# Optimization experiments

Hardware: AMD Instinct MI355X
Metric: run time of the kernel (lower is better)

Reference implementation:

```python
import jax, jax.numpy as jnp
import numpy as np

M_FUZZ = 2.0        # self.m
EPSILON = 1e-8      # self.Epsilon
MAX_ITER = 25       # self.max_iterion


def setup_inputs() -> dict:
    key = jax.random.key(0)
    k1, k2 = jax.random.split(key)
    data = jax.random.normal(k1, (300000, 64), dtype=jnp.float32)
    u0_raw = jax.random.uniform(k2, (300000, 64), dtype=jnp.float32)
    return {"data": data, "u0_raw": u0_raw, "cluster": 64}


def reference(data, u0_raw, cluster):
    # Fuzzy c-means, faithful to GranularComputing.forward:
    #   iterate: C = center(U); U = update(U, C); C_new = center(U);
    #            stop if ||C_new - C||_F < Epsilon; return C (pre-update center).
    m = M_FUZZ
    p = 2.0 / (m - 1.0)  # exponent in membership update (== 2.0)
    N, D = data.shape

    # initialize_matrix_U: random rows normalized to sum to 1
    U0 = u0_raw / jnp.sum(u0_raw, axis=1, keepdims=True)  # [N, c]

    def center(U):
        Um = U ** m                                        # [N, c]
        num = Um.T @ data                                  # [c, D]
        den = jnp.sum(Um, axis=0)[:, None]                 # [c, 1]
        return num / den

    x2 = jnp.sum(data * data, axis=1, keepdims=True)       # [N, 1]

    def sqdist(C):
        # squared Euclidean distances [N, c] via expansion (no N x c x D tensor)
        c2 = jnp.sum(C * C, axis=1)                        # [c]
        return jnp.maximum(x2 + c2 - 2.0 * (data @ C.T), 0.0)

    def step(carry, _):
        U, C_ret, done = carry
        C = center(U)                                      # [c, D]
        # u_ij = 1 / sum_k (d_ij / d_ik)^p  ==  d_ij^{-p} / sum_k d_ik^{-p}
        w = sqdist(C) ** (-p / 2.0)                        # [N, c]
        U_new = w / jnp.sum(w, axis=1, keepdims=True)
        C_new = center(U_new)
        diff = jnp.sqrt(jnp.sum((C_new - C) ** 2))
        # freeze state after convergence (emulates the early break)
        U_out = jnp.where(done, U, U_new)
        C_out = jnp.where(done, C_ret, C)
        return (U_out, C_out, done | (diff < EPSILON)), None

    C0 = jnp.zeros((cluster, D), dtype=data.dtype)
    (_, V, _), _ = jax.lax.scan(
        step, (U0, C0, jnp.array(False)), None, length=MAX_ITER + 1
    )
    return V  # [cluster, D]
```

## Files before the change

kernel.cpp:

```cpp
#include <hip/hip_runtime.h>


#define DM 64
#define CL 64
#define PARTIAL_STRIDE 4160
#define MAX_ITER 25
#define MAX_BLOCKS 512
#define LDP 72

typedef __attribute__((ext_vector_type(8))) short bf16x8;
typedef __attribute__((ext_vector_type(4))) float f32x4;

__device__ __forceinline__ unsigned f2bf1(float f) {
  unsigned u = __builtin_bit_cast(unsigned, f);
  return (u + 0x7FFFu + ((u >> 16) & 1u)) >> 16;
}
__device__ __forceinline__ unsigned pkbf(float a, float b) {
  return f2bf1(a) | (f2bf1(b) << 16);
}

__device__ __forceinline__ float wave_sum(float v) {
#define DPPADD(ctrl, rmask)                                                  \
  v += __builtin_bit_cast(float, __builtin_amdgcn_update_dpp(                \
           0, __builtin_bit_cast(int, v), ctrl, rmask, 0xf, false));
  DPPADD(0x111, 0xf)
  DPPADD(0x112, 0xf)
  DPPADD(0x114, 0xf)
  DPPADD(0x118, 0xf)
  DPPADD(0x142, 0xa)
  DPPADD(0x143, 0xc)
#undef DPPADD
  return __builtin_bit_cast(
      float, __builtin_amdgcn_readlane(__builtin_bit_cast(int, v), 63));
}

__device__ __forceinline__ float group16_sum(float v) {
#define DPPADD(ctrl)                                                         \
  v += __builtin_bit_cast(float, __builtin_amdgcn_update_dpp(                \
           0, __builtin_bit_cast(int, v), ctrl, 0xf, 0xf, false));
  DPPADD(0xB1)
  DPPADD(0x4E)
  DPPADD(0x141)
  DPPADD(0x140)
#undef DPPADD
  return v;
}

__global__ void fcm_prep(const float* __restrict__ data, float* __restrict__ x2,
                         unsigned short* __restrict__ xbf,
                         float* __restrict__ diffac, int* __restrict__ done,
                         int* __restrict__ ticket, int N) {
  int i = blockIdx.x * blockDim.x + threadIdx.x;
  if (i == 0) { *diffac = 0.0f; *done = 0; *ticket = 0; }
  if (i < N) {
    const float4* r = (const float4*)(data + (size_t)i * DM);
    unsigned short* xo = xbf + (size_t)i * DM;
    float s = 0.0f;
#pragma unroll
    for (int q = 0; q < DM / 4; q++) {
      float4 v = r[q];
      s = fmaf(v.x, v.x, s); s = fmaf(v.y, v.y, s);
      s = fmaf(v.z, v.z, s); s = fmaf(v.w, v.w, s);
      uint2 pk = {pkbf(v.x, v.y), pkbf(v.z, v.w)};
      *(uint2*)(void*)(xo + q * 4) = pk;
    }
    x2[i] = s;
  }
}

template <bool INIT>
__global__ __launch_bounds__(256, 3)
void fcm_pass(const unsigned short* __restrict__ xbf, const float* __restrict__ x2,
              const float* __restrict__ CU,
              float* __restrict__ partial, const int* __restrict__ done,
              int N, int ntiles) {
  if (!INIT && *done) return;
  __shared__ __align__(16) unsigned short Xb[64 * LDP];
  __shared__ __align__(16) unsigned short XTb[64 * LDP];
  __shared__ __align__(16) unsigned short umT[64 * LDP];
  __shared__ __align__(16) float rpart[4 * 64];
  __shared__ __align__(16) float rrs[64];
  __shared__ __align__(16) float x2s[64];

  const int tid  = threadIdx.x;
  const int w    = __builtin_amdgcn_readfirstlane(tid >> 6);
  const int col  = tid & 15;
  const int quad = (tid >> 4) & 3;

  bf16x8 cf0, cf1;
  float c2j = 0.0f;
  if (!INIT) {
    const float* crow = CU + (size_t)(16 * w + col) * DM;
    float4 ca = *(const float4*)(crow + quad * 8);
    float4 cb = *(const float4*)(crow + quad * 8 + 4);
    float4 cc = *(const float4*)(crow + 32 + quad * 8);
    float4 cd = *(const float4*)(crow + 32 + quad * 8 + 4);
    float cp = ca.x*ca.x + ca.y*ca.y + ca.z*ca.z + ca.w*ca.w
             + cb.x*cb.x + cb.y*cb.y + cb.z*cb.z + cb.w*cb.w
             + cc.x*cc.x + cc.y*cc.y + cc.z*cc.z + cc.w*cc.w
             + cd.x*cd.x + cd.y*cd.y + cd.z*cd.z + cd.w*cd.w;
    cp += __shfl_xor(cp, 16, 64);
    cp += __shfl_xor(cp, 32, 64);
    c2j = cp;
    union { bf16x8 v; unsigned u[4]; } P0, P1;
    P0.u[0] = pkbf(ca.x, ca.y); P0.u[1] = pkbf(ca.z, ca.w);
    P0.u[2] = pkbf(cb.x, cb.y); P0.u[3] = pkbf(cb.z, cb.w);
    P1.u[0] = pkbf(cc.x, cc.y); P1.u[1] = pkbf(cc.z, cc.w);
    P1.u[2] = pkbf(cd.x, cd.y); P1.u[3] = pkbf(cd.z, cd.w);
    cf0 = P0.v; cf1 = P1.v;
  }

  f32x4 D2[4];
#pragma unroll
  for (int dt = 0; dt < 4; dt++) D2[dt] = f32x4{0.f, 0.f, 0.f, 0.f};
  float den = 0.0f;

  for (int t = blockIdx.x; t < ntiles; t += gridDim.x) {
    const int base = t * 64;
    const int np = min(64, N - base);
    __syncthreads();

    for (int i = tid; i < 512; i += 256) {
      int p = i >> 3;
      int d8 = (i & 7) * 8;
      bf16x8 v = bf16x8{0, 0, 0, 0, 0, 0, 0, 0};
      if (p < np) v = *(const bf16x8*)(xbf + (size_t)(base + p) * DM + d8);
      *(bf16x8*)(void*)&Xb[p * LDP + d8] = v;
#pragma unroll
      for (int k = 0; k < 8; k++)
        XTb[(d8 + k) * LDP + p] = (unsigned short)v[k];
    }
    if (tid < 64) x2s[tid] = (base + tid < N) ? x2[base + tid] : 0.0f;
    __syncthreads();

    float W[4][4];
    if (INIT) {
#pragma unroll
      for (int pt = 0; pt < 4; pt++)
#pragma unroll
        for (int r = 0; r < 4; r++) {
          int pl = pt * 16 + quad * 4 + r;
          W[pt][r] = (pl < np)
              ? CU[(size_t)(base + pl) * CL + 16 * w + col] : 0.0f;
        }
    } else {
#pragma unroll
      for (int pt = 0; pt < 4; pt++) {
        bf16x8 a0 = *(const bf16x8*)(const void*)&Xb[(pt * 16 + col) * LDP + quad * 8];
        bf16x8 a1 = *(const bf16x8*)(const void*)&Xb[(pt * 16 + col) * LDP + 32 + quad * 8];
        f32x4 s = f32x4{0.f, 0.f, 0.f, 0.f};
        s = __builtin_amdgcn_mfma_f32_16x16x32_bf16(a0, cf0, s, 0, 0, 0);
        s = __builtin_amdgcn_mfma_f32_16x16x32_bf16(a1, cf1, s, 0, 0, 0);
        f32x4 x2v = *(const f32x4*)(const void*)&x2s[pt * 16 + quad * 4];
#pragma unroll
        for (int r = 0; r < 4; r++) {
          float dist = fmaxf(fmaf(-2.0f, s[r], x2v[r] + c2j), 0.0f);
          W[pt][r] = __builtin_amdgcn_rcpf(dist);
        }
      }
    }

    float rs[4][4];
#pragma unroll
    for (int pt = 0; pt < 4; pt++)
#pragma unroll
      for (int r = 0; r < 4; r++) rs[pt][r] = group16_sum(W[pt][r]);
    if (col == 0) {
#pragma unroll
      for (int pt = 0; pt < 4; pt++) {
        float4 v4 = {rs[pt][0], rs[pt][1], rs[pt][2], rs[pt][3]};
        *(float4*)(void*)&rpart[w * 64 + pt * 16 + quad * 4] = v4;
      }
    }
    __syncthreads();
    if (tid < 64) {
      float rt = rpart[tid] + rpart[64 + tid] + rpart[128 + tid] + rpart[192 + tid];
      rrs[tid] = __builtin_amdgcn_rcpf(rt);
    }
    __syncthreads();

#pragma unroll
    for (int pt = 0; pt < 4; pt++) {
      f32x4 rrv = *(const f32x4*)(const void*)&rrs[pt * 16 + quad * 4];
      float um[4];
#pragma unroll
      for (int r = 0; r < 4; r++) {
        float u = W[pt][r] * rrv[r];
        float m = u * u;
        um[r] = (pt * 16 + quad * 4 + r < np) ? m : 0.0f;
        den += um[r];
      }
      unsigned long long w64 = (unsigned long long)pkbf(um[0], um[1]) |
                               ((unsigned long long)pkbf(um[2], um[3]) << 32);
      *(unsigned long long*)(void*)&umT[(16 * w + col) * LDP + pt * 16 + quad * 4] = w64;
    }

#pragma unroll
    for (int pb = 0; pb < 2; pb++) {
      bf16x8 au = *(const bf16x8*)(const void*)&umT[(16 * w + col) * LDP + pb * 32 + quad * 8];
#pragma unroll
      for (int dt = 0; dt < 4; dt++) {
        bf16x8 bx = *(const bf16x8*)(const void*)&XTb[(dt * 16 + col) * LDP + pb * 32 + quad * 8];
        D2[dt] = __builtin_amdgcn_mfma_f32_16x16x32_bf16(au, bx, D2[dt], 0, 0, 0);
      }
    }
  }

  den += __shfl_xor(den, 16, 64);
  den += __shfl_xor(den, 32, 64);
  float* pb = partial + (size_t)blockIdx.x * PARTIAL_STRIDE;
  if (quad == 0) pb[CL * DM + 16 * w + col] = den;
#pragma unroll
  for (int dt = 0; dt < 4; dt++)
#pragma unroll
    for (int r = 0; r < 4; r++)
      pb[(size_t)(16 * w + quad * 4 + r) * DM + dt * 16 + col] = D2[dt][r];
}

__global__ __launch_bounds__(1024, 1)
void fcm_reduce(const float* __restrict__ partial, float* __restrict__ Cnew,
                const float* __restrict__ Cold, float* __restrict__ out,
                float* __restrict__ diffac, int* __restrict__ done,
                int* __restrict__ ticket, int compute_diff, int nb) {
  if (compute_diff && *done) return;
  __shared__ float sm[16 * 64];
  __shared__ float sden[1024];
  __shared__ int lastflag;
  __shared__ float sdiff;
  int j = blockIdx.x;
  int tid = threadIdx.x;
  int d = tid & 63;
  int slice = tid >> 6;
  float s = 0.0f;
  for (int b = slice; b < nb; b += 16)
    s += partial[(size_t)b * PARTIAL_STRIDE + j * DM + d];
  sm[slice * 64 + d] = s;
  float dv = 0.0f;
  for (int b = tid; b < nb; b += 1024)
    dv += partial[(size_t)b * PARTIAL_STRIDE + CL * DM + j];
  sden[tid] = dv;
  __syncthreads();
#pragma unroll
  for (int st = 8; st; st >>= 1) {
    if (slice < st) sm[slice * 64 + d] += sm[(slice + st) * 64 + d];
    __syncthreads();
  }
#pragma unroll
  for (int st = 512; st >= 64; st >>= 1) {
    if (tid < st) sden[tid] += sden[tid + st];
    __syncthreads();
  }
  if (tid < 64) {
    float denj = wave_sum(sden[tid]);
    float c = sm[tid] / denj;
    Cnew[j * DM + tid] = c;
    if (compute_diff) {
      float df = c - Cold[j * DM + tid];
      float tot = wave_sum(df * df);
      if (tid == 0) atomicAdd(diffac, tot);
    }
  }
  if (!compute_diff) return;
  __syncthreads();
  if (tid == 0) {
    __threadfence();
    int t = atomicAdd(ticket, 1);
    lastflag = (t == (int)gridDim.x - 1);
  }
  __syncthreads();
  if (!lastflag) return;
  if (tid == 0) sdiff = atomicAdd(diffac, 0.0f);
  __syncthreads();
  if (sdiff < 1e-16f) {
    for (int i = tid; i < CL * DM; i += 1024) out[i] = Cold[i];
    if (tid == 0) *done = 1;
  }
  if (tid == 0) { *diffac = 0.0f; *ticket = 0; }
}

__global__ void fcm_final(const float* __restrict__ Clast, float* __restrict__ out,
                          const int* __restrict__ done) {
  if (*done) return;
  int i = blockIdx.x * blockDim.x + threadIdx.x;
  if (i < CL * DM) out[i] = Clast[i];
}

extern "C" void kernel_launch(void* const* d_in, const int* in_sizes, int n_in,
                              void* d_out, int out_size, void* d_ws, size_t ws_size,
                              hipStream_t stream) {
  const float* data = (const float*)d_in[0];
  const float* u0   = (const float*)d_in[1];
  float* out = (float*)d_out;
  int N = in_sizes[0] / DM;
  int ntiles = (N + 63) / 64;

  float* ws = (float*)d_ws;
  size_t Noff = ((size_t)N + 15) & ~(size_t)15;
  float* x2 = ws;
  unsigned short* xbf = (unsigned short*)(ws + Noff);
  float* C0 = ws + Noff + (size_t)N * 32;
  float* C1 = C0 + CL * DM;
  float* diffac = C1 + CL * DM;
  int* done = (int*)(diffac + 1);
  int* ticket = (int*)(diffac + 2);
  float* partial = diffac + 16;

  size_t used = Noff + (size_t)N * 32 + 2 * CL * DM + 16;
  size_t avail = (ws_size / 4 > used) ? (ws_size / 4 - used) / PARTIAL_STRIDE : 0;
  int nb = (int)(avail < MAX_BLOCKS ? avail : MAX_BLOCKS);
  if (nb < 1) nb = 1;

  hipLaunchKernelGGL(fcm_prep, dim3((N + 255) / 256), dim3(256), 0, stream,
                     data, x2, xbf, diffac, done, ticket, N);
  hipLaunchKernelGGL((fcm_pass<true>), dim3(nb), dim3(256), 0, stream,
                     xbf, x2, u0, partial, done, N, ntiles);
  hipLaunchKernelGGL(fcm_reduce, dim3(64), dim3(1024), 0, stream,
                     partial, C0, C1, out, diffac, done, ticket, 0, nb);

  float* bufs[2] = {C0, C1};
  for (int k = 0; k < MAX_ITER; k++) {
    float* Cc = bufs[k & 1];
    float* Cn = bufs[(k + 1) & 1];
    hipLaunchKernelGGL((fcm_pass<false>), dim3(nb), dim3(256), 0, stream,
                       xbf, x2, Cc, partial, done, N, ntiles);
    hipLaunchKernelGGL(fcm_reduce, dim3(64), dim3(1024), 0, stream,
                       partial, Cn, Cc, out, diffac, done, ticket, 1, nb);
  }
  hipLaunchKernelGGL(fcm_final, dim3(16), dim3(256), 0, stream,
                     bufs[1], out, done);
}
```

Baseline: 427.1 us.

## Accumulate centers with global atomics and collapse reduce into single-block finalize

Each pass block now atomically adds its partial numerator and denominator sums into one shared accumulator, replacing the per-block partial buffers and the 64-block tree reduction with ticket counter. A one-block finalize divides, zeroes the accumulator, computes the convergence diff and writes the output on the last iteration, which also removes the separate final kernel. The prep kernel is reworked to 16 threads per row with a group reduction, and the transposed LDS tile is built from paired 32-bit loads instead of scalar 16-bit stores. The cost is atomic contention (512 blocks × 4160 atomics per pass) and nondeterministic float summation order.

Measured after the change: 1.635 ms. +282.8%, slower.

```diff
diff --git a/kernel.cpp b/kernel.cpp
--- a/kernel.cpp
+++ b/kernel.cpp
@@ -3,9 +3,8 @@
 
 #define DM 64
 #define CL 64
-#define PARTIAL_STRIDE 4160
 #define MAX_ITER 25
-#define MAX_BLOCKS 512
+#define NB 512
 #define LDP 72
 
 typedef __attribute__((ext_vector_type(8))) short bf16x8;
@@ -47,24 +46,20 @@
 }
 
 __global__ void fcm_prep(const float* __restrict__ data, float* __restrict__ x2,
-                         unsigned short* __restrict__ xbf,
-                         float* __restrict__ diffac, int* __restrict__ done,
-                         int* __restrict__ ticket, int N) {
-  int i = blockIdx.x * blockDim.x + threadIdx.x;
-  if (i == 0) { *diffac = 0.0f; *done = 0; *ticket = 0; }
-  if (i < N) {
-    const float4* r = (const float4*)(data + (size_t)i * DM);
-    unsigned short* xo = xbf + (size_t)i * DM;
-    float s = 0.0f;
-#pragma unroll
-    for (int q = 0; q < DM / 4; q++) {
-      float4 v = r[q];
-      s = fmaf(v.x, v.x, s); s = fmaf(v.y, v.y, s);
-      s = fmaf(v.z, v.z, s); s = fmaf(v.w, v.w, s);
-      uint2 pk = {pkbf(v.x, v.y), pkbf(v.z, v.w)};
-      *(uint2*)(void*)(xo + q * 4) = pk;
-    }
-    x2[i] = s;
+                         unsigned short* __restrict__ xbf, float* __restrict__ acc,
+                         int* __restrict__ done, int N) {
+  int g = blockIdx.x * blockDim.x + threadIdx.x;
+  if (g < CL * DM + CL) acc[g] = 0.0f;
+  if (g == CL * DM + CL) *done = 0;
+  int row = g >> 4;
+  int c = g & 15;
+  if (row < N) {
+    float4 v = *(const float4*)(data + (size_t)row * DM + c * 4);
+    float s = fmaf(v.x, v.x, fmaf(v.y, v.y, fmaf(v.z, v.z, v.w * v.w)));
+    s = group16_sum(s);
+    if (c == 0) x2[row] = s;
+    uint2 pk = {pkbf(v.x, v.y), pkbf(v.z, v.w)};
+    *(uint2*)(void*)(xbf + (size_t)row * DM + c * 4) = pk;
   }
 }
 
@@ -72,7 +67,7 @@
 __global__ __launch_bounds__(256, 3)
 void fcm_pass(const unsigned short* __restrict__ xbf, const float* __restrict__ x2,
               const float* __restrict__ CU,
-              float* __restrict__ partial, const int* __restrict__ done,
+              float* __restrict__ acc, const int* __restrict__ done,
               int N, int ntiles) {
   if (!INIT && *done) return;
   __shared__ __align__(16) unsigned short Xb[64 * LDP];
@@ -126,9 +121,19 @@
       bf16x8 v = bf16x8{0, 0, 0, 0, 0, 0, 0, 0};
       if (p < np) v = *(const bf16x8*)(xbf + (size_t)(base + p) * DM + d8);
       *(bf16x8*)(void*)&Xb[p * LDP + d8] = v;
-#pragma unroll
-      for (int k = 0; k < 8; k++)
-        XTb[(d8 + k) * LDP + p] = (unsigned short)v[k];
+    }
+#pragma unroll
+    for (int it = 0; it < 4; it++) {
+      int idx = it * 256 + tid;
+      int d = (idx >> 5) * 2;
+      int p = (idx & 31) * 2;
+      unsigned w0 = 0, w1 = 0;
+      if (p < np)     w0 = *(const unsigned*)(xbf + (size_t)(base + p) * DM + d);
+      if (p + 1 < np) w1 = *(const unsigned*)(xbf + (size_t)(base + p + 1) * DM + d);
+      unsigned t0 = (w0 & 0xFFFFu) | (w1 << 16);
+      unsigned t1 = (w0 >> 16) | (w1 & 0xFFFF0000u);
+      *(unsigned*)(void*)&XTb[d * LDP + p] = t0;
+      *(unsigned*)(void*)&XTb[(d + 1) * LDP + p] = t1;
     }
     if (tid < 64) x2s[tid] = (base + tid < N) ? x2[base + tid] : 0.0f;
     __syncthreads();
@@ -208,81 +213,48 @@
 
   den += __shfl_xor(den, 16, 64);
   den += __shfl_xor(den, 32, 64);
-  float* pb = partial + (size_t)blockIdx.x * PARTIAL_STRIDE;
-  if (quad == 0) pb[CL * DM + 16 * w + col] = den;
+  if (quad == 0) atomicAdd(&acc[CL * DM + 16 * w + col], den);
 #pragma unroll
   for (int dt = 0; dt < 4; dt++)
 #pragma unroll
     for (int r = 0; r < 4; r++)
-      pb[(size_t)(16 * w + quad * 4 + r) * DM + dt * 16 + col] = D2[dt][r];
-}
-
-__global__ __launch_bounds__(1024, 1)
-void fcm_reduce(const float* __restrict__ partial, float* __restrict__ Cnew,
-                const float* __restrict__ Cold, float* __restrict__ out,
-                float* __restrict__ diffac, int* __restrict__ done,
-                int* __restrict__ ticket, int compute_diff, int nb) {
+      atomicAdd(&acc[(size_t)(16 * w + quad * 4 + r) * DM + dt * 16 + col], D2[dt][r]);
+}
+
+__global__ __launch_bounds__(256)
+void fcm_finalize(float* __restrict__ acc, float* __restrict__ Cnew,
+                  const float* __restrict__ Cold, float* __restrict__ out,
+                  int* __restrict__ done, int compute_diff, int last) {
   if (compute_diff && *done) return;
-  __shared__ float sm[16 * 64];
-  __shared__ float sden[1024];
-  __shared__ int lastflag;
+  __shared__ float sden[64];
+  __shared__ float sdf[4];
   __shared__ float sdiff;
-  int j = blockIdx.x;
   int tid = threadIdx.x;
-  int d = tid & 63;
-  int slice = tid >> 6;
-  float s = 0.0f;
-  for (int b = slice; b < nb; b += 16)
-    s += partial[(size_t)b * PARTIAL_STRIDE + j * DM + d];
-  sm[slice * 64 + d] = s;
-  float dv = 0.0f;
-  for (int b = tid; b < nb; b += 1024)
-    dv += partial[(size_t)b * PARTIAL_STRIDE + CL * DM + j];
-  sden[tid] = dv;
+  if (tid < 64) { sden[tid] = acc[CL * DM + tid]; acc[CL * DM + tid] = 0.0f; }
   __syncthreads();
-#pragma unroll
-  for (int st = 8; st; st >>= 1) {
-    if (slice < st) sm[slice * 64 + d] += sm[(slice + st) * 64 + d];
-    __syncthreads();
-  }
-#pragma unroll
-  for (int st = 512; st >= 64; st >>= 1) {
-    if (tid < st) sden[tid] += sden[tid + st];
-    __syncthreads();
-  }
-  if (tid < 64) {
-    float denj = wave_sum(sden[tid]);
-    float c = sm[tid] / denj;
-    Cnew[j * DM + tid] = c;
-    if (compute_diff) {
-      float df = c - Cold[j * DM + tid];
-      float tot = wave_sum(df * df);
-      if (tid == 0) atomicAdd(diffac, tot);
-    }
+  float dsum = 0.0f;
+#pragma unroll
+  for (int q = 0; q < 16; q++) {
+    int idx = q * 256 + tid;
+    float c = acc[idx] / sden[idx >> 6];
+    acc[idx] = 0.0f;
+    Cnew[idx] = c;
+    if (compute_diff) { float df = c - Cold[idx]; dsum = fmaf(df, df, dsum); }
   }
   if (!compute_diff) return;
+  dsum = wave_sum(dsum);
+  if ((tid & 63) == 0) sdf[tid >> 6] = dsum;
   __syncthreads();
-  if (tid == 0) {
-    __threadfence();
-    int t = atomicAdd(ticket, 1);
-    lastflag = (t == (int)gridDim.x - 1);
-  }
-  __syncthreads();
-  if (!lastflag) return;
-  if (tid == 0) sdiff = atomicAdd(diffac, 0.0f);
+  if (tid == 0) sdiff = (sdf[0] + sdf[1]) + (sdf[2] + sdf[3]);
   __syncthreads();
   if (sdiff < 1e-16f) {
-    for (int i = tid; i < CL * DM; i += 1024) out[i] = Cold[i];
+#pragma unroll
+    for (int q = 0; q < 16; q++) out[q * 256 + tid] = Cold[q * 256 + tid];
     if (tid == 0) *done = 1;
-  }
-  if (tid == 0) { *diffac = 0.0f; *ticket = 0; }
-}
-
-__global__ void fcm_final(const float* __restrict__ Clast, float* __restrict__ out,
-                          const int* __restrict__ done) {
-  if (*done) return;
-  int i = blockIdx.x * blockDim.x + threadIdx.x;
-  if (i < CL * DM) out[i] = Clast[i];
+  } else if (last) {
+#pragma unroll
+    for (int q = 0; q < 16; q++) out[q * 256 + tid] = Cnew[q * 256 + tid];
+  }
 }
 
 extern "C" void kernel_launch(void* const* d_in, const int* in_sizes, int n_in,
@@ -300,32 +272,23 @@
   unsigned short* xbf = (unsigned short*)(ws + Noff);
   float* C0 = ws + Noff + (size_t)N * 32;
   float* C1 = C0 + CL * DM;
-  float* diffac = C1 + CL * DM;
-  int* done = (int*)(diffac + 1);
-  int* ticket = (int*)(diffac + 2);
-  float* partial = diffac + 16;
-
-  size_t used = Noff + (size_t)N * 32 + 2 * CL * DM + 16;
-  size_t avail = (ws_size / 4 > used) ? (ws_size / 4 - used) / PARTIAL_STRIDE : 0;
-  int nb = (int)(avail < MAX_BLOCKS ? avail : MAX_BLOCKS);
-  if (nb < 1) nb = 1;
-
-  hipLaunchKernelGGL(fcm_prep, dim3((N + 255) / 256), dim3(256), 0, stream,
-                     data, x2, xbf, diffac, done, ticket, N);
-  hipLaunchKernelGGL((fcm_pass<true>), dim3(nb), dim3(256), 0, stream,
-                     xbf, x2, u0, partial, done, N, ntiles);
-  hipLaunchKernelGGL(fcm_reduce, dim3(64), dim3(1024), 0, stream,
-                     partial, C0, C1, out, diffac, done, ticket, 0, nb);
+  float* acc = C1 + CL * DM;
+  int* done = (int*)(acc + CL * DM + CL);
+
+  hipLaunchKernelGGL(fcm_prep, dim3((N * 16 + 255) / 256), dim3(256), 0, stream,
+                     data, x2, xbf, acc, done, N);
+  hipLaunchKernelGGL((fcm_pass<true>), dim3(NB), dim3(256), 0, stream,
+                     xbf, x2, u0, acc, done, N, ntiles);
+  hipLaunchKernelGGL(fcm_finalize, dim3(1), dim3(256), 0, stream,
+                     acc, C0, C1, out, done, 0, 0);
 
   float* bufs[2] = {C0, C1};
   for (int k = 0; k < MAX_ITER; k++) {
     float* Cc = bufs[k & 1];
     float* Cn = bufs[(k + 1) & 1];
-    hipLaunchKernelGGL((fcm_pass<false>), dim3(nb), dim3(256), 0, stream,
-                       xbf, x2, Cc, partial, done, N, ntiles);
-    hipLaunchKernelGGL(fcm_reduce, dim3(64), dim3(1024), 0, stream,
-                       partial, Cn, Cc, out, diffac, done, ticket, 1, nb);
-  }
-  hipLaunchKernelGGL(fcm_final, dim3(16), dim3(256), 0, stream,
-                     bufs[1], out, done);
-}
+    hipLaunchKernelGGL((fcm_pass<false>), dim3(NB), dim3(256), 0, stream,
+                       xbf, x2, Cc, acc, done, N, ntiles);
+    hipLaunchKernelGGL(fcm_finalize, dim3(1), dim3(256), 0, stream,
+                       acc, Cn, Cc, out, done, 1, (k == MAX_ITER - 1) ? 1 : 0);
+  }
+}
```

## Remap waves to point rows to drop cross-wave row-sum sync; coalesce prep and transpose

Applied to the files above, without the earlier changes.

Each wave now owns 16 data points and all 64 clusters, holding all four centroid fragments in registers. The membership row sum can then be reduced inside the wave, which removes the shared-memory rpart/rrs round trip and two block barriers per tile. The XT transpose is rebuilt with paired 32-bit loads and stores in place of scalar 16-bit scattered writes. The prep kernel uses 16 threads per row for coalesced access, and the grid cap grows to 768 blocks. In exchange each thread holds more registers for the centroid fragments, which may reduce occupancy.

Result: no change. 430.3 us (+0.8%).

```diff
diff --git a/kernel.cpp b/kernel.cpp
--- a/kernel.cpp
+++ b/kernel.cpp
@@ -5,7 +5,7 @@
 #define CL 64
 #define PARTIAL_STRIDE 4160
 #define MAX_ITER 25
-#define MAX_BLOCKS 512
+#define MAX_BLOCKS 768
 #define LDP 72
 
 typedef __attribute__((ext_vector_type(8))) short bf16x8;
@@ -47,24 +47,19 @@
 }
 
 __global__ void fcm_prep(const float* __restrict__ data, float* __restrict__ x2,
-                         unsigned short* __restrict__ xbf,
-                         float* __restrict__ diffac, int* __restrict__ done,
-                         int* __restrict__ ticket, int N) {
-  int i = blockIdx.x * blockDim.x + threadIdx.x;
-  if (i == 0) { *diffac = 0.0f; *done = 0; *ticket = 0; }
-  if (i < N) {
-    const float4* r = (const float4*)(data + (size_t)i * DM);
-    unsigned short* xo = xbf + (size_t)i * DM;
-    float s = 0.0f;
-#pragma unroll
-    for (int q = 0; q < DM / 4; q++) {
-      float4 v = r[q];
-      s = fmaf(v.x, v.x, s); s = fmaf(v.y, v.y, s);
-      s = fmaf(v.z, v.z, s); s = fmaf(v.w, v.w, s);
-      uint2 pk = {pkbf(v.x, v.y), pkbf(v.z, v.w)};
-      *(uint2*)(void*)(xo + q * 4) = pk;
-    }
-    x2[i] = s;
+                         unsigned short* __restrict__ xbf, float* __restrict__ diffac,
+                         int* __restrict__ done, int* __restrict__ ticket, int N) {
+  int g = blockIdx.x * blockDim.x + threadIdx.x;
+  if (g == 0) { *diffac = 0.0f; *done = 0; *ticket = 0; }
+  int row = g >> 4;
+  int c = g & 15;
+  if (row < N) {
+    float4 v = *(const float4*)(data + (size_t)row * DM + c * 4);
+    float s = fmaf(v.x, v.x, fmaf(v.y, v.y, fmaf(v.z, v.z, v.w * v.w)));
+    s = group16_sum(s);
+    if (c == 0) x2[row] = s;
+    uint2 pk = {pkbf(v.x, v.y), pkbf(v.z, v.w)};
+    *(uint2*)(void*)(xbf + (size_t)row * DM + c * 4) = pk;
   }
 }
 
@@ -79,7 +74,6 @@
   __shared__ __align__(16) unsigned short XTb[64 * LDP];
   __shared__ __align__(16) unsigned short umT[64 * LDP];
   __shared__ __align__(16) float rpart[4 * 64];
-  __shared__ __align__(16) float rrs[64];
   __shared__ __align__(16) float x2s[64];
 
   const int tid  = threadIdx.x;
@@ -87,33 +81,36 @@
   const int col  = tid & 15;
   const int quad = (tid >> 4) & 3;
 
-  bf16x8 cf0, cf1;
-  float c2j = 0.0f;
+  bf16x8 cf[4][2];
+  float c2v[4];
   if (!INIT) {
-    const float* crow = CU + (size_t)(16 * w + col) * DM;
-    float4 ca = *(const float4*)(crow + quad * 8);
-    float4 cb = *(const float4*)(crow + quad * 8 + 4);
-    float4 cc = *(const float4*)(crow + 32 + quad * 8);
-    float4 cd = *(const float4*)(crow + 32 + quad * 8 + 4);
-    float cp = ca.x*ca.x + ca.y*ca.y + ca.z*ca.z + ca.w*ca.w
-             + cb.x*cb.x + cb.y*cb.y + cb.z*cb.z + cb.w*cb.w
-             + cc.x*cc.x + cc.y*cc.y + cc.z*cc.z + cc.w*cc.w
-             + cd.x*cd.x + cd.y*cd.y + cd.z*cd.z + cd.w*cd.w;
-    cp += __shfl_xor(cp, 16, 64);
-    cp += __shfl_xor(cp, 32, 64);
-    c2j = cp;
-    union { bf16x8 v; unsigned u[4]; } P0, P1;
-    P0.u[0] = pkbf(ca.x, ca.y); P0.u[1] = pkbf(ca.z, ca.w);
-    P0.u[2] = pkbf(cb.x, cb.y); P0.u[3] = pkbf(cb.z, cb.w);
-    P1.u[0] = pkbf(cc.x, cc.y); P1.u[1] = pkbf(cc.z, cc.w);
-    P1.u[2] = pkbf(cd.x, cd.y); P1.u[3] = pkbf(cd.z, cd.w);
-    cf0 = P0.v; cf1 = P1.v;
+#pragma unroll
+    for (int g = 0; g < 4; g++) {
+      const float* crow = CU + (size_t)(g * 16 + col) * DM;
+      float4 ca = *(const float4*)(crow + quad * 8);
+      float4 cb = *(const float4*)(crow + quad * 8 + 4);
+      float4 cc = *(const float4*)(crow + 32 + quad * 8);
+      float4 cd = *(const float4*)(crow + 32 + quad * 8 + 4);
+      float cp = ca.x*ca.x + ca.y*ca.y + ca.z*ca.z + ca.w*ca.w
+               + cb.x*cb.x + cb.y*cb.y + cb.z*cb.z + cb.w*cb.w
+               + cc.x*cc.x + cc.y*cc.y + cc.z*cc.z + cc.w*cc.w
+               + cd.x*cd.x + cd.y*cd.y + cd.z*cd.z + cd.w*cd.w;
+      cp += __shfl_xor(cp, 16, 64);
+      cp += __shfl_xor(cp, 32, 64);
+      c2v[g] = cp;
+      union { bf16x8 v; unsigned u[4]; } P0, P1;
+      P0.u[0] = pkbf(ca.x, ca.y); P0.u[1] = pkbf(ca.z, ca.w);
+      P0.u[2] = pkbf(cb.x, cb.y); P0.u[3] = pkbf(cb.z, cb.w);
+      P1.u[0] = pkbf(cc.x, cc.y); P1.u[1] = pkbf(cc.z, cc.w);
+      P1.u[2] = pkbf(cd.x, cd.y); P1.u[3] = pkbf(cd.z, cd.w);
+      cf[g][0] = P0.v; cf[g][1] = P1.v;
+    }
   }
 
   f32x4 D2[4];
 #pragma unroll
   for (int dt = 0; dt < 4; dt++) D2[dt] = f32x4{0.f, 0.f, 0.f, 0.f};
-  float den = 0.0f;
+  float denacc[4] = {0.f, 0.f, 0.f, 0.f};
 
   for (int t = blockIdx.x; t < ntiles; t += gridDim.x) {
     const int base = t * 64;
@@ -126,9 +123,19 @@
       bf16x8 v = bf16x8{0, 0, 0, 0, 0, 0, 0, 0};
       if (p < np) v = *(const bf16x8*)(xbf + (size_t)(base + p) * DM + d8);
       *(bf16x8*)(void*)&Xb[p * LDP + d8] = v;
-#pragma unroll
-      for (int k = 0; k < 8; k++)
-        XTb[(d8 + k) * LDP + p] = (unsigned short)v[k];
+    }
+#pragma unroll
+    for (int it = 0; it < 4; it++) {
+      int idx = it * 256 + tid;
+      int d = (idx >> 5) * 2;
+      int p = (idx & 31) * 2;
+      unsigned w0 = 0, w1 = 0;
+      if (p < np)     w0 = *(const unsigned*)(xbf + (size_t)(base + p) * DM + d);
+      if (p + 1 < np) w1 = *(const unsigned*)(xbf + (size_t)(base + p + 1) * DM + d);
+      unsigned t0 = (w0 & 0xFFFFu) | (w1 << 16);
+      unsigned t1 = (w0 >> 16) | (w1 & 0xFFFF0000u);
+      *(unsigned*)(void*)&XTb[d * LDP + p] = t0;
+      *(unsigned*)(void*)&XTb[(d + 1) * LDP + p] = t1;
     }
     if (tid < 64) x2s[tid] = (base + tid < N) ? x2[base + tid] : 0.0f;
     __syncthreads();
@@ -136,64 +143,52 @@
     float W[4][4];
     if (INIT) {
 #pragma unroll
-      for (int pt = 0; pt < 4; pt++)
+      for (int g = 0; g < 4; g++)
 #pragma unroll
         for (int r = 0; r < 4; r++) {
-          int pl = pt * 16 + quad * 4 + r;
-          W[pt][r] = (pl < np)
-              ? CU[(size_t)(base + pl) * CL + 16 * w + col] : 0.0f;
+          int pl = 16 * w + quad * 4 + r;
+          W[g][r] = (pl < np)
+              ? CU[(size_t)(base + pl) * CL + g * 16 + col] : 0.0f;
         }
     } else {
-#pragma unroll
-      for (int pt = 0; pt < 4; pt++) {
-        bf16x8 a0 = *(const bf16x8*)(const void*)&Xb[(pt * 16 + col) * LDP + quad * 8];
-        bf16x8 a1 = *(const bf16x8*)(const void*)&Xb[(pt * 16 + col) * LDP + 32 + quad * 8];
+      bf16x8 a0 = *(const bf16x8*)(const void*)&Xb[(16 * w + col) * LDP + quad * 8];
+      bf16x8 a1 = *(const bf16x8*)(const void*)&Xb[(16 * w + col) * LDP + 32 + quad * 8];
+      f32x4 x2v = *(const f32x4*)(const void*)&x2s[16 * w + quad * 4];
+#pragma unroll
+      for (int g = 0; g < 4; g++) {
         f32x4 s = f32x4{0.f, 0.f, 0.f, 0.f};
-        s = __builtin_amdgcn_mfma_f32_16x16x32_bf16(a0, cf0, s, 0, 0, 0);
-        s = __builtin_amdgcn_mfma_f32_16x16x32_bf16(a1, cf1, s, 0, 0, 0);
-        f32x4 x2v = *(const f32x4*)(const void*)&x2s[pt * 16 + quad * 4];
+        s = __builtin_amdgcn_mfma_f32_16x16x32_bf16(a0, cf[g][0], s, 0, 0, 0);
+        s = __builtin_amdgcn_mfma_f32_16x16x32_bf16(a1, cf[g][1], s, 0, 0, 0);
 #pragma unroll
         for (int r = 0; r < 4; r++) {
-          float dist = fmaxf(fmaf(-2.0f, s[r], x2v[r] + c2j), 0.0f);
-          W[pt][r] = __builtin_amdgcn_rcpf(dist);
+          float dist = fmaxf(fmaf(-2.0f, s[r], x2v[r] + c2v[g]), 0.0f);
+          W[g][r] = __builtin_amdgcn_rcpf(dist);
         }
       }
     }
 
-    float rs[4][4];
-#pragma unroll
-    for (int pt = 0; pt < 4; pt++)
-#pragma unroll
-      for (int r = 0; r < 4; r++) rs[pt][r] = group16_sum(W[pt][r]);
-    if (col == 0) {
-#pragma unroll
-      for (int pt = 0; pt < 4; pt++) {
-        float4 v4 = {rs[pt][0], rs[pt][1], rs[pt][2], rs[pt][3]};
-        *(float4*)(void*)&rpart[w * 64 + pt * 16 + quad * 4] = v4;
+    float rr[4];
+#pragma unroll
+    for (int r = 0; r < 4; r++) {
+      float s = (W[0][r] + W[1][r]) + (W[2][r] + W[3][r]);
+      rr[r] = __builtin_amdgcn_rcpf(group16_sum(s));
+    }
+
+#pragma unroll
+    for (int g = 0; g < 4; g++) {
+      float um[4];
+#pragma unroll
+      for (int r = 0; r < 4; r++) {
+        float u = W[g][r] * rr[r];
+        float m = u * u;
+        um[r] = (16 * w + quad * 4 + r < np) ? m : 0.0f;
       }
-    }
-    __syncthreads();
-    if (tid < 64) {
-      float rt = rpart[tid] + rpart[64 + tid] + rpart[128 + tid] + rpart[192 + tid];
-      rrs[tid] = __builtin_amdgcn_rcpf(rt);
-    }
-    __syncthreads();
-
-#pragma unroll
-    for (int pt = 0; pt < 4; pt++) {
-      f32x4 rrv = *(const f32x4*)(const void*)&rrs[pt * 16 + quad * 4];
-      float um[4];
-#pragma unroll
-      for (int r = 0; r < 4; r++) {
-        float u = W[pt][r] * rrv[r];
-        float m = u * u;
-        um[r] = (pt * 16 + quad * 4 + r < np) ? m : 0.0f;
-        den += um[r];
-      }
+      denacc[g] += ((um[0] + um[1]) + (um[2] + um[3]));
       unsigned long long w64 = (unsigned long long)pkbf(um[0], um[1]) |
                                ((unsigned long long)pkbf(um[2], um[3]) << 32);
-      *(unsigned long long*)(void*)&umT[(16 * w + col) * LDP + pt * 16 + quad * 4] = w64;
-    }
+      *(unsigned long long*)(void*)&umT[(g * 16 + col) * LDP + 16 * w + quad * 4] = w64;
+    }
+    __syncthreads();
 
 #pragma unroll
     for (int pb = 0; pb < 2; pb++) {
@@ -206,10 +201,17 @@
     }
   }
 
-  den += __shfl_xor(den, 16, 64);
-  den += __shfl_xor(den, 32, 64);
+#pragma unroll
+  for (int g = 0; g < 4; g++) {
+    float dv = denacc[g];
+    dv += __shfl_xor(dv, 16, 64);
+    dv += __shfl_xor(dv, 32, 64);
+    if (quad == 0) rpart[w * 64 + g * 16 + col] = dv;
+  }
+  __syncthreads();
   float* pb = partial + (size_t)blockIdx.x * PARTIAL_STRIDE;
-  if (quad == 0) pb[CL * DM + 16 * w + col] = den;
+  if (tid < 64)
+    pb[CL * DM + tid] = (rpart[tid] + rpart[64 + tid]) + (rpart[128 + tid] + rpart[192 + tid]);
 #pragma unroll
   for (int dt = 0; dt < 4; dt++)
 #pragma unroll
@@ -310,7 +312,7 @@
   int nb = (int)(avail < MAX_BLOCKS ? avail : MAX_BLOCKS);
   if (nb < 1) nb = 1;
 
-  hipLaunchKernelGGL(fcm_prep, dim3((N + 255) / 256), dim3(256), 0, stream,
+  hipLaunchKernelGGL(fcm_prep, dim3((N * 16 + 255) / 256), dim3(256), 0, stream,
                      data, x2, xbf, diffac, done, ticket, N);
   hipLaunchKernelGGL((fcm_pass<true>), dim3(nb), dim3(256), 0, stream,
                      xbf, x2, u0, partial, done, N, ntiles);
```
